# Kernel tuning notes

Measured on AMD Instinct MI355X. Metric: run time of the kernel, lower is better.

Reference implementation:

```python
import jax, jax.numpy as jnp
import numpy as np

B, N, E, R = 2, 4096, 1024, 128   # batch, seq_len, embed_dim, expand_ratio (head_dim)
H = E // R                        # num heads (scalar decay per head)
EPS = 1e-5                        # torch LayerNorm default eps


def _silu(x):
    return x * jax.nn.sigmoid(x)


def setup_inputs() -> dict:
    key = jax.random.key(0)
    ks = jax.random.split(key, 12)
    std = 0.02

    def w(k, shape):
        return jax.random.normal(k, shape, jnp.float32) * std

    return {
        "x": jax.random.normal(ks[0], (B, N, E), jnp.float32),
        # log of lower bound of the decay gate; must be negative so exp() in (0,1)
        "log_lower_bound": -jax.random.uniform(ks[1], (H,), jnp.float32, minval=0.1, maxval=3.0),
        "Wq": w(ks[2], (E, E)),
        "Wk": w(ks[3], (E, E)),
        "Wv": w(ks[4], (E, E)),
        "Wf": w(ks[5], (H, E)),      # f_proj: embed_dim -> embed_dim // expand_ratio
        "Wb1": w(ks[6], (R, E)),     # bet_proj low-rank
        "Wb2": w(ks[7], (E, R)),
        "Wg1": w(ks[8], (R, E)),     # output_gate low-rank
        "Wg2": w(ks[9], (E, R)),
        "gamma": jnp.ones((E,), jnp.float32),  # LayerNorm weight (bias=False)
        "Wo": w(ks[10], (E, E)),
    }


def _simple_gla(q, k, v, g):
    """Gated linear attention recurrence (fla simple_gla semantics).
    q,k,v: [B,H,N,R]; g: [B,H,N] (log decay per head per step).
    S_t = exp(g_t) * S_{t-1} + k_t v_t^T ;  o_t = (q_t * d^-0.5) @ S_t
    """
    scale = q.shape[-1] ** -0.5
    qT = jnp.moveaxis(q, 2, 0)  # [N,B,H,R]
    kT = jnp.moveaxis(k, 2, 0)
    vT = jnp.moveaxis(v, 2, 0)
    gT = jnp.moveaxis(g, 2, 0)  # [N,B,H]

    S0 = jnp.zeros((q.shape[0], q.shape[1], q.shape[-1], v.shape[-1]), q.dtype)

    def step(S, inp):
        qt, kt, vt, gt = inp
        S = S * jnp.exp(gt)[..., None, None] + kt[..., :, None] * vt[..., None, :]
        o = jnp.einsum('bhk,bhkv->bhv', qt * scale, S)
        return S, o

    _, o = jax.lax.scan(step, S0, (qT, kT, vT, gT))
    return jnp.moveaxis(o, 0, 2)  # [B,H,N,R]


def reference(x, log_lower_bound, Wq, Wk, Wv, Wf, Wb1, Wb2, Wg1, Wg2, gamma, Wo):
    # projections + activations
    q = _silu(x @ Wq.T)
    k = _silu(x @ Wk.T)
    v = x @ Wv.T
    f = x @ Wf.T                      # [B,N,H] scalar decay logits per head

    # householder q-transform with dense-memory beta (normalized reflection vector)
    beta = _silu((x @ Wb1.T) @ Wb2.T)  # [B,N,E]
    bn = beta * jax.lax.rsqrt(jnp.sum(beta * beta, -1, keepdims=True) + 1e-12)
    q = q - 2.0 * jnp.sum(q * bn, -1, keepdims=True) * bn

    def split_heads(t):  # [B,N,E] -> [B,H,N,R]
        return jnp.moveaxis(t.reshape(B, N, H, R), 2, 1)

    qh, kh, vh = split_heads(q), split_heads(k), split_heads(v)

    # log-space decay gate with lower bound
    lb = jnp.exp(log_lower_bound)                      # [H] in (0,1)
    fg = lb + (1.0 - lb) * jax.nn.sigmoid(f)           # [B,N,H]
    log_f = jnp.transpose(jnp.log(fg), (0, 2, 1))      # [B,H,N]

    o = _simple_gla(qh, kh, vh, log_f)                 # [B,H,N,R]
    o = jnp.moveaxis(o, 1, 2).reshape(B, N, E)

    # output gate
    gate = jax.nn.sigmoid((x @ Wg1.T) @ Wg2.T)
    o = o * gate

    # LayerNorm (weight only, bias=False)
    mu = jnp.mean(o, -1, keepdims=True)
    var = jnp.mean((o - mu) ** 2, -1, keepdims=True)
    o = (o - mu) * jax.lax.rsqrt(var + EPS) * gamma

    return o @ Wo.T
```

## Files before the change

kernel.cpp:

```cpp
#include <hip/hip_runtime.h>
#include <hip/hip_bf16.h>

using u16 = unsigned short;
typedef __attribute__((ext_vector_type(8))) short bf16x8;
typedef __attribute__((ext_vector_type(4))) float f32x4;
typedef __attribute__((ext_vector_type(8))) u16 u16x8;
typedef __attribute__((ext_vector_type(4))) u16 u16x4;

#define B_ 2
#define N_ 4096
#define E_ 1024
#define R_ 128
#define H_ 8
#define M_ 8192
#define CHUNK_ 128
#define NC_ 32
#define BH_ 16

__device__ __forceinline__ float b2f(u16 u) { return __uint_as_float(((unsigned)u) << 16); }
__device__ __forceinline__ u16 f2b(float f) {
  unsigned u = __float_as_uint(f);
  return (u16)((u + 0x7fffu + ((u >> 16) & 1u)) >> 16);
}
__device__ __forceinline__ float sigm(float x) {
  return __builtin_amdgcn_rcpf(1.0f + __expf(-x));
}

#define GLDS(g, l) __builtin_amdgcn_global_load_lds( \
    (const __attribute__((address_space(1))) unsigned int*)(g), \
    (__attribute__((address_space(3))) unsigned int*)(l), 16, 0, 0)

struct CvtArgs {
  const float* src[10];
  u16* dst[11];
};

__global__ void __launch_bounds__(256) cvt_all(CvtArgs a) {
  int idx = blockIdx.x * 256 + threadIdx.x;
  const int SZ[11] = {2097152, 262144, 262144, 262144, 2048,
                      32768, 32768, 32768, 32768, 262144, 30720};
  int off = idx, seg = 0;
#pragma unroll
  for (int i = 0; i < 10; i++) {
    if (seg == i && off >= SZ[i]) { off -= SZ[i]; seg = i + 1; }
  }
  u16x4 z = (u16x4){0, 0, 0, 0};
  if (seg == 10) { ((u16x4*)a.dst[10])[off] = z; return; }
  float4 v = ((const float4*)a.src[seg])[off];
  u16x4 r;
  r[0] = f2b(v.x); r[1] = f2b(v.y); r[2] = f2b(v.z); r[3] = f2b(v.w);
  if (seg == 6) {
    int n = off >> 5, c = off & 31;
    u16x4* W2 = (u16x4*)a.dst[6];
    W2[n * 64 + c] = r; W2[n * 64 + 32 + c] = z;
  } else if (seg == 8) {
    int n = off >> 5, c = off & 31;
    u16x4* W2 = (u16x4*)a.dst[8];
    W2[(1024 + n) * 64 + 32 + c] = r; W2[(1024 + n) * 64 + c] = z;
  } else {
    ((u16x4*)a.dst[seg])[off] = r;
  }
}

template<bool SWAP>
__device__ __forceinline__ void mfma_panel(f32x4 (&acc)[4][4], const u16* A, const u16* Bm,
                                           int wr, int wc, int l15, int q8) {
  bf16x8 af[4], bf[4];
#pragma unroll
  for (int mi = 0; mi < 4; mi++) af[mi] = *(const bf16x8*)&A[(wr * 64 + mi * 16 + l15) * 32 + q8];
#pragma unroll
  for (int ni = 0; ni < 4; ni++) bf[ni] = *(const bf16x8*)&Bm[(wc * 64 + ni * 16 + l15) * 32 + q8];
#pragma unroll
  for (int mi = 0; mi < 4; mi++)
#pragma unroll
    for (int ni = 0; ni < 4; ni++)
      acc[mi][ni] = SWAP
        ? __builtin_amdgcn_mfma_f32_16x16x32_bf16(bf[ni], af[mi], acc[mi][ni], 0, 0, 0)
        : __builtin_amdgcn_mfma_f32_16x16x32_bf16(af[mi], bf[ni], acc[mi][ni], 0, 0, 0);
}

template<bool SWAP, int K>
__device__ __forceinline__ void gemm_loop(const u16* __restrict__ X, const u16* __restrict__ W,
                                          int m0, int n0,
                                          u16* As, u16* Bs, f32x4 (&acc)[4][4], int tid) {
  const int wave = tid >> 6, lane = tid & 63;
  const int wr = wave >> 1, wc = wave & 1, l15 = lane & 15, q8 = (lane >> 4) * 8;
  const u16* Ap = X + (size_t)(m0 + wave * 32 + (lane >> 2)) * K + (lane & 3) * 8;
  const u16* Bp = W + (size_t)(n0 + wave * 32 + (lane >> 2)) * K + (lane & 3) * 8;
  u16* A0 = As + wave * 1024;
  u16* B0 = Bs + wave * 1024;
#pragma unroll
  for (int k0 = 0; k0 < K; k0 += 64) {
    GLDS(Ap + k0,                    A0);
    GLDS(Ap + 16 * (size_t)K + k0,   A0 + 512);
    GLDS(Ap + k0 + 32,               A0 + 4096);
    GLDS(Ap + 16 * (size_t)K + k0 + 32, A0 + 4608);
    GLDS(Bp + k0,                    B0);
    GLDS(Bp + 16 * (size_t)K + k0,   B0 + 512);
    GLDS(Bp + k0 + 32,               B0 + 4096);
    GLDS(Bp + 16 * (size_t)K + k0 + 32, B0 + 4608);
    __syncthreads();
    mfma_panel<SWAP>(acc, As, Bs, wr, wc, l15, q8);
    mfma_panel<SWAP>(acc, As + 4096, Bs + 4096, wr, wc, l15, q8);
    __syncthreads();
  }
}

template<bool SWAP>
__device__ __forceinline__ void gemm128_dbuf(const u16* __restrict__ X, const u16* __restrict__ W,
                                             int m0, int n0, u16* sh, f32x4 (&acc)[4][4], int tid) {
  const int w = tid >> 6, lane = tid & 63;
  const int wr = w >> 1, wc = w & 1;
  const int l15 = lane & 15, g = lane >> 4;
  const int lrow = tid >> 2;
  const int scol = (tid & 3) ^ ((lrow ^ (lrow >> 2)) & 3);
  const u16* pA0 = X + (size_t)(m0 + lrow) * 1024 + scol * 8;
  const u16* pA1 = X + (size_t)(m0 + 64 + lrow) * 1024 + scol * 8;
  const u16* pB0 = W + (size_t)(n0 + lrow) * 1024 + scol * 8;
  const u16* pB1 = W + (size_t)(n0 + 64 + lrow) * 1024 + scol * 8;
  const int sw = (g ^ (l15 & 3) ^ ((l15 >> 2) & 3)) << 4;
  const int abase = (wr * 64 + l15) * 64 + sw;
  const int bbase = (wc * 64 + l15) * 64 + sw;

#define STG128(T, bi) do {                                                      \
    char* Ad_ = (char*)sh + (bi) * 16384;                                       \
    char* Bd_ = (char*)sh + 8192 + (bi) * 16384;                                \
    GLDS(pA0 + (size_t)(T) * 32, Ad_ + w * 1024);                               \
    GLDS(pA1 + (size_t)(T) * 32, Ad_ + 4096 + w * 1024);                        \
    GLDS(pB0 + (size_t)(T) * 32, Bd_ + w * 1024);                               \
    GLDS(pB1 + (size_t)(T) * 32, Bd_ + 4096 + w * 1024);                        \
  } while (0)

  STG128(0, 0);
  __syncthreads();

#pragma unroll 2
  for (int t = 0; t < 32; ++t) {
    if (t < 31) STG128(t + 1, (t + 1) & 1);
    const char* Ab = (const char*)sh + (t & 1) * 16384;
    const char* Bb = (const char*)sh + 8192 + (t & 1) * 16384;
    bf16x8 af[4], bf[4];
#pragma unroll
    for (int mi = 0; mi < 4; mi++) af[mi] = *(const bf16x8*)(Ab + abase + mi * 1024);
#pragma unroll
    for (int ni = 0; ni < 4; ni++) bf[ni] = *(const bf16x8*)(Bb + bbase + ni * 1024);
    __builtin_amdgcn_s_setprio(1);
#pragma unroll
    for (int mi = 0; mi < 4; mi++)
#pragma unroll
      for (int ni = 0; ni < 4; ni++)
        acc[mi][ni] = SWAP
          ? __builtin_amdgcn_mfma_f32_16x16x32_bf16(bf[ni], af[mi], acc[mi][ni], 0, 0, 0)
          : __builtin_amdgcn_mfma_f32_16x16x32_bf16(af[mi], bf[ni], acc[mi][ni], 0, 0, 0);
    __builtin_amdgcn_s_setprio(0);
    __syncthreads();
  }
#undef STG128
}

__global__ void __launch_bounds__(256, 4) mega_gemm(const u16* __restrict__ X, const u16* __restrict__ Wcat,
                                                    const float* __restrict__ llb,
                                                    u16* __restrict__ Qb, u16* __restrict__ Kb,
                                                    u16* __restrict__ KT, u16* __restrict__ VT,
                                                    u16* __restrict__ T1, float* __restrict__ LOGF) {
  __shared__ u16 sh[17408];
  u16* Ts = sh;
  const int tid = threadIdx.x;
  const int m0 = blockIdx.y * 128;
  const int ny = blockIdx.x, n0 = ny * 128;
  const int wave = tid >> 6, lane = tid & 63;
  const int wr = wave >> 1, wc = wave & 1, l15 = lane & 15, q4 = (lane >> 4) * 4;
  f32x4 acc[4][4];
#pragma unroll
  for (int i = 0; i < 4; i++)
#pragma unroll
    for (int j = 0; j < 4; j++) acc[i][j] = (f32x4){0.f, 0.f, 0.f, 0.f};

  if (ny >= 16 && ny < 24) {
    gemm128_dbuf<false>(X, Wcat, m0, n0, sh, acc, tid);
#pragma unroll
    for (int mi = 0; mi < 4; mi++) {
#pragma unroll
      for (int ni = 0; ni < 4; ni++) {
        int col = n0 - 2048 + wc * 64 + ni * 16 + l15;
        int rbase = m0 + wr * 64 + mi * 16 + q4;
        int head = col >> 7, rl = col & 127;
        int bb = rbase >> 12, nseq = rbase & (N_ - 1);
        u16x4 pk;
#pragma unroll
        for (int r = 0; r < 4; r++) pk[r] = f2b(acc[mi][ni][r]);
        *(u16x4*)&VT[((size_t)(bb * H_ + head) * R_ + rl) * N_ + nseq] = pk;
      }
    }
    return;
  }

  gemm128_dbuf<true>(X, Wcat, m0, n0, sh, acc, tid);

  if (ny == 26) {
    if (wc == 0 && (lane >> 4) < 2) {
#pragma unroll
      for (int mi = 0; mi < 4; mi++) {
        int mcol = m0 + wr * 64 + mi * 16 + l15;
        int bb = mcol >> 12, nseq = mcol & (N_ - 1);
#pragma unroll
        for (int r = 0; r < 4; r++) {
          int h = q4 + r;
          float lb = __expf(llb[h]);
          LOGF[(size_t)(bb * H_ + h) * N_ + nseq] =
              __logf(lb + (1.f - lb) * sigm(acc[mi][0][r]));
        }
      }
    }
    return;
  }

#pragma unroll
  for (int mi = 0; mi < 4; mi++) {
#pragma unroll
    for (int ni = 0; ni < 4; ni++) {
      int nb = n0 + wc * 64 + ni * 16 + q4;
      int mcol = m0 + wr * 64 + mi * 16 + l15;
      u16x4 pk;
#pragma unroll
      for (int r = 0; r < 4; r++) {
        float v = acc[mi][ni][r];
        if (ny < 16) v = v * sigm(v);
        pk[r] = f2b(v);
      }
      if (ny < 8) {
        *(u16x4*)&Qb[(size_t)mcol * E_ + nb] = pk;
      } else if (ny < 16) {
        *(u16x4*)&Kb[(size_t)mcol * E_ + nb - 1024] = pk;
        int nl = nb - n0;
        int ml = mcol - m0;
#pragma unroll
        for (int r = 0; r < 4; r++) Ts[(nl + r) * 136 + ml] = pk[r];
      } else {
        *(u16x4*)&T1[(size_t)mcol * 256 + nb - 3072] = pk;
      }
    }
  }

  if (ny >= 8 && ny < 16) {
    __syncthreads();
    int head = (n0 - 1024) >> 7;
    int bb = m0 >> 12, nloc = m0 & (N_ - 1);
    size_t base = ((size_t)(bb * H_ + head) * R_) * N_ + nloc;
#pragma unroll
    for (int p = 0; p < 8; p++) {
      int nl = p * 16 + (tid >> 4);
      int m8 = (tid & 15) * 8;
      u16x8 v = *(const u16x8*)&Ts[nl * 136 + m8];
      *(u16x8*)&KT[base + (size_t)nl * N_ + m8] = v;
    }
  }
}

__global__ void __launch_bounds__(256) bg_gemm(const u16* __restrict__ T1, const u16* __restrict__ W2,
                                               u16* __restrict__ BETA, u16* __restrict__ GATE) {
  __shared__ u16 As[8192];
  __shared__ u16 Bs[8192];
  const int tid = threadIdx.x;
  const int m0 = blockIdx.x * 128;
  const int n0 = blockIdx.y * 128;
  f32x4 acc[4][4];
#pragma unroll
  for (int i = 0; i < 4; i++)
#pragma unroll
    for (int j = 0; j < 4; j++) acc[i][j] = (f32x4){0.f, 0.f, 0.f, 0.f};
  gemm_loop<true, 256>(T1, W2, m0, n0, As, Bs, acc, tid);
  const int wave = tid >> 6, lane = tid & 63;
  const int wr = wave >> 1, wc = wave & 1, l15 = lane & 15, q4 = (lane >> 4) * 4;
#pragma unroll
  for (int mi = 0; mi < 4; mi++) {
#pragma unroll
    for (int ni = 0; ni < 4; ni++) {
      int nb = n0 + wc * 64 + ni * 16 + q4;
      int mcol = m0 + wr * 64 + mi * 16 + l15;
      u16x4 pk;
      if (nb < 1024) {
#pragma unroll
        for (int r = 0; r < 4; r++) {
          float v = acc[mi][ni][r];
          pk[r] = f2b(v * sigm(v));
        }
        *(u16x4*)&BETA[(size_t)mcol * E_ + nb] = pk;
      } else {
#pragma unroll
        for (int r = 0; r < 4; r++) pk[r] = f2b(sigm(acc[mi][ni][r]));
        *(u16x4*)&GATE[(size_t)mcol * E_ + nb - 1024] = pk;
      }
    }
  }
}

__global__ void __launch_bounds__(256) out_gemm(const u16* __restrict__ X, const u16* __restrict__ W,
                                                float* __restrict__ C) {
  __shared__ u16 As[8192];
  __shared__ u16 Bs[8192];
  const int tid = threadIdx.x;
  const int m0 = blockIdx.x * 128;
  const int n0 = blockIdx.y * 128;
  f32x4 acc[4][4];
#pragma unroll
  for (int i = 0; i < 4; i++)
#pragma unroll
    for (int j = 0; j < 4; j++) acc[i][j] = (f32x4){0.f, 0.f, 0.f, 0.f};
  gemm_loop<true, 1024>(X, W, m0, n0, As, Bs, acc, tid);
  const int wave = tid >> 6, lane = tid & 63;
  const int wr = wave >> 1, wc = wave & 1, l15 = lane & 15, q4 = (lane >> 4) * 4;
#pragma unroll
  for (int mi = 0; mi < 4; mi++) {
#pragma unroll
    for (int ni = 0; ni < 4; ni++) {
      int nb = n0 + wc * 64 + ni * 16 + q4;
      int mcol = m0 + wr * 64 + mi * 16 + l15;
      *(f32x4*)&C[(size_t)mcol * E_ + nb] = acc[mi][ni];
    }
  }
}

__global__ void __launch_bounds__(256) householder(u16* __restrict__ Q, const u16* __restrict__ BETA) {
  int row = blockIdx.x;
  int tid = threadIdx.x;
  u16* q = Q + (size_t)row * E_;
  const u16* bt = BETA + (size_t)row * E_;
  u16x4 q4 = *(const u16x4*)(q + tid * 4);
  u16x4 b4 = *(const u16x4*)(bt + tid * 4);
  float qv[4], bv[4];
#pragma unroll
  for (int i = 0; i < 4; i++) { qv[i] = b2f(q4[i]); bv[i] = b2f(b4[i]); }
  float ss = bv[0]*bv[0] + bv[1]*bv[1] + bv[2]*bv[2] + bv[3]*bv[3];
  float qd = qv[0]*bv[0] + qv[1]*bv[1] + qv[2]*bv[2] + qv[3]*bv[3];
  __shared__ float red[8];
#pragma unroll
  for (int m = 1; m < 64; m <<= 1) { ss += __shfl_xor(ss, m); qd += __shfl_xor(qd, m); }
  int wid = tid >> 6;
  if ((tid & 63) == 0) { red[wid] = ss; red[4 + wid] = qd; }
  __syncthreads();
  ss = red[0] + red[1] + red[2] + red[3];
  qd = red[4] + red[5] + red[6] + red[7];
  float coef = 2.f * qd / (ss + 1e-12f);
  const float scale = 0.08838834764831845f;
  u16x4 o4;
#pragma unroll
  for (int i = 0; i < 4; i++) o4[i] = f2b((qv[i] - coef * bv[i]) * scale);
  *(u16x4*)(q + tid * 4) = o4;
}

__device__ __forceinline__ void scan_chunk(const float* __restrict__ lf, float* cum, int tid) {
  if (tid < 64) {
    float a = lf[tid], b = lf[tid + 64];
#pragma unroll
    for (int off = 1; off < 64; off <<= 1) {
      float t = __shfl_up(a, off);  if (tid >= off) a += t;
      float t2 = __shfl_up(b, off); if (tid >= off) b += t2;
    }
    b += __shfl(a, 63);
    cum[tid] = a; cum[tid + 64] = b;
  }
  __syncthreads();
}

__device__ __forceinline__ void stage32(u16* dst, const u16* src, size_t stride, int tid) {
  int r0 = tid >> 2, c8 = (tid & 3) * 8;
  *(u16x8*)&dst[(size_t)r0 * 40 + c8] = *(const u16x8*)&src[(size_t)r0 * stride + c8];
  int r1 = r0 + 64;
  *(u16x8*)&dst[(size_t)r1 * 40 + c8] = *(const u16x8*)&src[(size_t)r1 * stride + c8];
}

__device__ __forceinline__ void stage32_scaled(u16* dst, const u16* src, size_t stride,
                                               const float* w, int j0, int tid) {
  int c8 = (tid & 3) * 8;
  float wv[8];
#pragma unroll
  for (int i = 0; i < 8; i++) wv[i] = w[j0 + c8 + i];
#pragma unroll
  for (int rr = 0; rr < 128; rr += 64) {
    int r = rr + (tid >> 2);
    u16x8 raw = *(const u16x8*)&src[(size_t)r * stride + c8];
    u16x8 o;
#pragma unroll
    for (int i = 0; i < 8; i++) o[i] = f2b(b2f(raw[i]) * wv[i]);
    *(u16x8*)&dst[(size_t)r * 40 + c8] = o;
  }
}

template<bool SWAP>
__device__ __forceinline__ void mfma16(f32x4 (&acc)[4][4], const u16* A, const u16* Bm,
                                       int wr, int wc, int l15, int q8) {
  bf16x8 af[4], bf[4];
#pragma unroll
  for (int mi = 0; mi < 4; mi++) af[mi] = *(const bf16x8*)&A[(wr * 64 + mi * 16 + l15) * 40 + q8];
#pragma unroll
  for (int ni = 0; ni < 4; ni++) bf[ni] = *(const bf16x8*)&Bm[(wc * 64 + ni * 16 + l15) * 40 + q8];
#pragma unroll
  for (int mi = 0; mi < 4; mi++)
#pragma unroll
    for (int ni = 0; ni < 4; ni++)
      acc[mi][ni] = SWAP
        ? __builtin_amdgcn_mfma_f32_16x16x32_bf16(bf[ni], af[mi], acc[mi][ni], 0, 0, 0)
        : __builtin_amdgcn_mfma_f32_16x16x32_bf16(af[mi], bf[ni], acc[mi][ni], 0, 0, 0);
}

__global__ void __launch_bounds__(256) gla_phaseA(const u16* __restrict__ KT, const u16* __restrict__ VT,
                                                  const float* __restrict__ LOGF,
                                                  u16* __restrict__ U, float* __restrict__ DC) {
  const int blk = blockIdx.x;
  const int bh = blk >> 5, c = blk & 31;
  const int tid = threadIdx.x;
  const int wave = tid >> 6, lane = tid & 63;
  const int wr = wave >> 1, wc = wave & 1, l15 = lane & 15, q8 = (lane >> 4) * 8;
  __shared__ u16 SA[128 * 40];
  __shared__ u16 SB[128 * 40];
  __shared__ float cum[CHUNK_];
  __shared__ float wd[CHUNK_];
  scan_chunk(LOGF + (size_t)bh * N_ + c * CHUNK_, cum, tid);
  if (tid < 128) wd[tid] = __expf(cum[127] - cum[tid]);
  __syncthreads();
  const u16* vbase = VT + ((size_t)bh * R_) * N_ + (size_t)c * CHUNK_;
  const u16* kbase = KT + ((size_t)bh * R_) * N_ + (size_t)c * CHUNK_;
  f32x4 acc[4][4];
#pragma unroll
  for (int i = 0; i < 4; i++)
#pragma unroll
    for (int j = 0; j < 4; j++) acc[i][j] = (f32x4){0.f, 0.f, 0.f, 0.f};
  for (int j0 = 0; j0 < CHUNK_; j0 += 32) {
    __syncthreads();
    stage32(SA, vbase + j0, N_, tid);
    stage32_scaled(SB, kbase + j0, N_, wd, j0, tid);
    __syncthreads();
    mfma16<true>(acc, SA, SB, wr, wc, l15, q8);
  }
  u16* Up = U + (size_t)blk * (R_ * R_);
  const int q4 = (lane >> 4) * 4;
#pragma unroll
  for (int mi = 0; mi < 4; mi++) {
#pragma unroll
    for (int ni = 0; ni < 4; ni++) {
      int v = wr * 64 + mi * 16 + l15;
      int kb = wc * 64 + ni * 16 + q4;
      u16x4 pk;
#pragma unroll
      for (int r = 0; r < 4; r++) pk[r] = f2b(acc[mi][ni][r]);
      *(u16x4*)&Up[(size_t)v * R_ + kb] = pk;
    }
  }
  if (tid == 0) DC[blk] = __expf(cum[127]);
}

__global__ void __launch_bounds__(256) gla_phaseB(const u16* __restrict__ U, const float* __restrict__ DC,
                                                  u16* __restrict__ SSb) {
  int idx = blockIdx.x * 256 + threadIdx.x;
  int bh = idx >> 14;
  int e = idx & 16383;
  float s = 0.f;
  for (int c = 0; c < NC_; c++) {
    size_t off = ((size_t)bh * NC_ + c) * 16384 + e;
    SSb[off] = f2b(s);
    s = DC[bh * NC_ + c] * s + b2f(U[off]);
  }
}

__global__ void __launch_bounds__(256) gla_phaseC(const u16* __restrict__ Qb, const u16* __restrict__ Kb,
                                                  const u16* __restrict__ VT, const u16* __restrict__ SSb,
                                                  const float* __restrict__ LOGF, u16* __restrict__ Ob) {
  const int blk = blockIdx.x;
  const int bh = blk >> 5, c = blk & 31;
  const int b = bh >> 3, h = bh & 7;
  const int tid = threadIdx.x;
  const int wave = tid >> 6, lane = tid & 63;
  const int wr = wave >> 1, wc = wave & 1, l15 = lane & 15;
  const int q4i = (lane >> 4) * 4, q8 = (lane >> 4) * 8;
  __shared__ u16 SA[128 * 40];
  __shared__ u16 SB[128 * 40];
  __shared__ u16 Ps[128 * 136];
  __shared__ float cum[CHUNK_];
  __shared__ float cumE[CHUNK_];
  scan_chunk(LOGF + (size_t)bh * N_ + c * CHUNK_, cum, tid);
  if (tid < 128) cumE[tid] = __expf(cum[tid]);
  __syncthreads();
  const size_t rowbase = ((size_t)(b * N_ + c * CHUNK_)) * E_ + (size_t)h * R_;
  const u16* vtbase = VT + ((size_t)bh * R_) * N_ + (size_t)c * CHUNK_;
  const u16* ssbase = SSb + (size_t)blk * (R_ * R_);

  f32x4 acc[4][4];
#pragma unroll
  for (int i = 0; i < 4; i++)
#pragma unroll
    for (int j = 0; j < 4; j++) acc[i][j] = (f32x4){0.f, 0.f, 0.f, 0.f};

  for (int r0 = 0; r0 < R_; r0 += 32) {
    __syncthreads();
    stage32(SA, Kb + rowbase + r0, E_, tid);
    stage32(SB, Qb + rowbase + r0, E_, tid);
    __syncthreads();
    mfma16<false>(acc, SA, SB, wr, wc, l15, q8);
  }
#pragma unroll
  for (int mi = 0; mi < 4; mi++) {
#pragma unroll
    for (int ni = 0; ni < 4; ni++) {
      int jb = wr * 64 + mi * 16 + q4i;
      int i = wc * 64 + ni * 16 + l15;
      float ci = cum[i];
      float4 cj = *(const float4*)&cum[jb];
      u16x4 pk;
      float cjv[4] = {cj.x, cj.y, cj.z, cj.w};
#pragma unroll
      for (int r = 0; r < 4; r++) {
        int j = jb + r;
        float w = (j <= i) ? __expf(ci - cjv[r]) : 0.f;
        pk[r] = f2b(acc[mi][ni][r] * w);
      }
      *(u16x4*)&Ps[i * 136 + jb] = pk;
    }
  }
#pragma unroll
  for (int i = 0; i < 4; i++)
#pragma unroll
    for (int j = 0; j < 4; j++) acc[i][j] = (f32x4){0.f, 0.f, 0.f, 0.f};
  for (int k0 = 0; k0 < R_; k0 += 32) {
    __syncthreads();
    stage32(SA, Qb + rowbase + k0, E_, tid);
    stage32(SB, ssbase + k0, R_, tid);
    __syncthreads();
    mfma16<true>(acc, SA, SB, wr, wc, l15, q8);
  }
#pragma unroll
  for (int mi = 0; mi < 4; mi++) {
    float ei = cumE[wr * 64 + mi * 16 + l15];
#pragma unroll
    for (int ni = 0; ni < 4; ni++)
#pragma unroll
      for (int r = 0; r < 4; r++) acc[mi][ni][r] *= ei;
  }
  for (int j0 = 0; j0 < CHUNK_; j0 += 32) {
    __syncthreads();
    stage32(SB, vtbase + j0, N_, tid);
    __syncthreads();
    if (wr == 1 || j0 < 64) {
      bf16x8 af[4], bf[4];
#pragma unroll
      for (int mi = 0; mi < 4; mi++)
        af[mi] = *(const bf16x8*)&Ps[(wr * 64 + mi * 16 + l15) * 136 + j0 + q8];
#pragma unroll
      for (int ni = 0; ni < 4; ni++)
        bf[ni] = *(const bf16x8*)&SB[(wc * 64 + ni * 16 + l15) * 40 + q8];
#pragma unroll
      for (int mi = 0; mi < 4; mi++)
#pragma unroll
        for (int ni = 0; ni < 4; ni++)
          acc[mi][ni] = __builtin_amdgcn_mfma_f32_16x16x32_bf16(bf[ni], af[mi], acc[mi][ni], 0, 0, 0);
    }
  }
#pragma unroll
  for (int mi = 0; mi < 4; mi++) {
#pragma unroll
    for (int ni = 0; ni < 4; ni++) {
      int i = wr * 64 + mi * 16 + l15;
      int vb = wc * 64 + ni * 16 + q4i;
      u16x4 pk;
#pragma unroll
      for (int r = 0; r < 4; r++) pk[r] = f2b(acc[mi][ni][r]);
      *(u16x4*)&Ob[rowbase + (size_t)i * E_ + vb] = pk;
    }
  }
}

__global__ void __launch_bounds__(256) gate_ln(const u16* __restrict__ O, const u16* __restrict__ G,
                                               const float* __restrict__ gamma, u16* __restrict__ OLN) {
  int row = blockIdx.x, tid = threadIdx.x;
  u16x4 o4 = *(const u16x4*)(O + (size_t)row * E_ + tid * 4);
  u16x4 g4 = *(const u16x4*)(G + (size_t)row * E_ + tid * 4);
  float x0 = b2f(o4[0]) * b2f(g4[0]), x1 = b2f(o4[1]) * b2f(g4[1]);
  float x2 = b2f(o4[2]) * b2f(g4[2]), x3 = b2f(o4[3]) * b2f(g4[3]);
  float s = x0 + x1 + x2 + x3;
  float sq = x0 * x0 + x1 * x1 + x2 * x2 + x3 * x3;
  __shared__ float red[8];
#pragma unroll
  for (int m = 1; m < 64; m <<= 1) { s += __shfl_xor(s, m); sq += __shfl_xor(sq, m); }
  int wid = tid >> 6;
  if ((tid & 63) == 0) { red[wid] = s; red[4 + wid] = sq; }
  __syncthreads();
  s = red[0] + red[1] + red[2] + red[3];
  sq = red[4] + red[5] + red[6] + red[7];
  float mu = s * (1.f / 1024.f);
  float var = sq * (1.f / 1024.f) - mu * mu;
  float rs = rsqrtf(var + 1e-5f);
  int e = tid * 4;
  u16x4 r4;
  r4[0] = f2b((x0 - mu) * rs * gamma[e + 0]);
  r4[1] = f2b((x1 - mu) * rs * gamma[e + 1]);
  r4[2] = f2b((x2 - mu) * rs * gamma[e + 2]);
  r4[3] = f2b((x3 - mu) * rs * gamma[e + 3]);
  *(u16x4*)(OLN + (size_t)row * E_ + e) = r4;
}

extern "C" void kernel_launch(void* const* d_in, const int* in_sizes, int n_in,
                              void* d_out, int out_size, void* d_ws, size_t ws_size,
                              hipStream_t stream) {
  (void)in_sizes; (void)n_in; (void)out_size; (void)ws_size;
  const float* x   = (const float*)d_in[0];
  const float* llb = (const float*)d_in[1];
  const float* Wq  = (const float*)d_in[2];
  const float* Wk  = (const float*)d_in[3];
  const float* Wv  = (const float*)d_in[4];
  const float* Wf  = (const float*)d_in[5];
  const float* Wb1 = (const float*)d_in[6];
  const float* Wb2 = (const float*)d_in[7];
  const float* Wg1 = (const float*)d_in[8];
  const float* Wg2 = (const float*)d_in[9];
  const float* gm  = (const float*)d_in[10];
  const float* Wo  = (const float*)d_in[11];
  float* out = (float*)d_out;

  char* ws = (char*)d_ws;
  const size_t SZB = (size_t)M_ * E_ * 2;
  u16*   Qb    = (u16*)(ws + 0 * SZB);
  u16*   Kb    = (u16*)(ws + 1 * SZB);
  u16*   KT    = (u16*)(ws + 2 * SZB);
  u16*   VT    = (u16*)(ws + 3 * SZB);
  u16*   BETAb = (u16*)(ws + 4 * SZB);
  u16*   GATEb = (u16*)(ws + 5 * SZB);
  u16*   SSb   = (u16*)(ws + 6 * SZB);
  u16*   XB    = (u16*)(ws + 7 * SZB);
  u16*   U     = (u16*)(ws + 8 * SZB);
  char*  tail  = ws + 8 * SZB + (size_t)BH_ * NC_ * R_ * R_ * 2;
  u16*   Wcat  = (u16*)tail;
  u16*   Wcat2 = Wcat + (size_t)3456 * 1024;
  u16*   WOb   = Wcat2 + (size_t)2048 * 256;
  u16*   T1    = WOb + (size_t)E_ * E_;
  float* LOGF  = (float*)(T1 + (size_t)M_ * 256);
  float* DC    = LOGF + (size_t)BH_ * N_;
  u16*   Ob    = BETAb;
  u16*   OLN   = Qb;

  CvtArgs ca;
  ca.src[0] = x;   ca.dst[0]  = XB;
  ca.src[1] = Wq;  ca.dst[1]  = Wcat;
  ca.src[2] = Wk;  ca.dst[2]  = Wcat + (size_t)1024 * 1024;
  ca.src[3] = Wv;  ca.dst[3]  = Wcat + (size_t)2048 * 1024;
  ca.src[4] = Wf;  ca.dst[4]  = Wcat + (size_t)3328 * 1024;
  ca.src[5] = Wb1; ca.dst[5]  = Wcat + (size_t)3072 * 1024;
  ca.src[6] = Wb2; ca.dst[6]  = Wcat2;
  ca.src[7] = Wg1; ca.dst[7]  = Wcat + (size_t)3200 * 1024;
  ca.src[8] = Wg2; ca.dst[8]  = Wcat2;
  ca.src[9] = Wo;  ca.dst[9]  = WOb;
  ca.dst[10] = Wcat + (size_t)3336 * 1024;

  dim3 blk(256);
  cvt_all<<<dim3(12928), blk, 0, stream>>>(ca);
  mega_gemm<<<dim3(27, 64), blk, 0, stream>>>(XB, Wcat, llb, Qb, Kb, KT, VT, T1, LOGF);
  bg_gemm<<<dim3(64, 16), blk, 0, stream>>>(T1, Wcat2, BETAb, GATEb);
  householder<<<dim3(M_), blk, 0, stream>>>(Qb, BETAb);
  gla_phaseA<<<dim3(BH_ * NC_), blk, 0, stream>>>(KT, VT, LOGF, U, DC);
  gla_phaseB<<<dim3(BH_ * 16384 / 256), blk, 0, stream>>>(U, DC, SSb);
  gla_phaseC<<<dim3(BH_ * NC_), blk, 0, stream>>>(Qb, Kb, VT, SSb, LOGF, Ob);
  gate_ln<<<dim3(M_), blk, 0, stream>>>(Ob, GATEb, gm, OLN);
  out_gemm<<<dim3(64, 8), blk, 0, stream>>>(OLN, WOb, out);
}
```

Before: 310.1 us.

## Swap GEMM loops between kernels and double-buffer chunk-attention staging

Makes the double-buffered 128-tile GEMM generic over K and uses it in bg_gemm and out_gemm, each now tagged with an occupancy hint of 4. mega_gemm goes back to the simpler single-buffered gemm_loop and loses its occupancy hint. The chunk-state and chunk-output kernels now stage their 32-wide slices into two alternating shared buffers, so the next slice's global load overlaps the current MFMA work and one barrier per step is removed. The cost is more shared memory per block in the attention kernels, which may lower occupancy, and mega_gemm no longer overlaps its loads with compute.

```diff
diff --git a/kernel.cpp b/kernel.cpp
--- a/kernel.cpp
+++ b/kernel.cpp
@@ -106,7 +106,7 @@
   }
 }
 
-template<bool SWAP>
+template<bool SWAP, int K>
 __device__ __forceinline__ void gemm128_dbuf(const u16* __restrict__ X, const u16* __restrict__ W,
                                              int m0, int n0, u16* sh, f32x4 (&acc)[4][4], int tid) {
   const int w = tid >> 6, lane = tid & 63;
@@ -114,10 +114,10 @@
   const int l15 = lane & 15, g = lane >> 4;
   const int lrow = tid >> 2;
   const int scol = (tid & 3) ^ ((lrow ^ (lrow >> 2)) & 3);
-  const u16* pA0 = X + (size_t)(m0 + lrow) * 1024 + scol * 8;
-  const u16* pA1 = X + (size_t)(m0 + 64 + lrow) * 1024 + scol * 8;
-  const u16* pB0 = W + (size_t)(n0 + lrow) * 1024 + scol * 8;
-  const u16* pB1 = W + (size_t)(n0 + 64 + lrow) * 1024 + scol * 8;
+  const u16* pA0 = X + (size_t)(m0 + lrow) * K + scol * 8;
+  const u16* pA1 = X + (size_t)(m0 + 64 + lrow) * K + scol * 8;
+  const u16* pB0 = W + (size_t)(n0 + lrow) * K + scol * 8;
+  const u16* pB1 = W + (size_t)(n0 + 64 + lrow) * K + scol * 8;
   const int sw = (g ^ (l15 & 3) ^ ((l15 >> 2) & 3)) << 4;
   const int abase = (wr * 64 + l15) * 64 + sw;
   const int bbase = (wc * 64 + l15) * 64 + sw;
@@ -135,8 +135,8 @@
   __syncthreads();
 
 #pragma unroll 2
-  for (int t = 0; t < 32; ++t) {
-    if (t < 31) STG128(t + 1, (t + 1) & 1);
+  for (int t = 0; t < K / 32; ++t) {
+    if (t < K / 32 - 1) STG128(t + 1, (t + 1) & 1);
     const char* Ab = (const char*)sh + (t & 1) * 16384;
     const char* Bb = (const char*)sh + 8192 + (t & 1) * 16384;
     bf16x8 af[4], bf[4];
@@ -158,12 +158,14 @@
 #undef STG128
 }
 
-__global__ void __launch_bounds__(256, 4) mega_gemm(const u16* __restrict__ X, const u16* __restrict__ Wcat,
-                                                    const float* __restrict__ llb,
-                                                    u16* __restrict__ Qb, u16* __restrict__ Kb,
-                                                    u16* __restrict__ KT, u16* __restrict__ VT,
-                                                    u16* __restrict__ T1, float* __restrict__ LOGF) {
+__global__ void __launch_bounds__(256) mega_gemm(const u16* __restrict__ X, const u16* __restrict__ Wcat,
+                                                 const float* __restrict__ llb,
+                                                 u16* __restrict__ Qb, u16* __restrict__ Kb,
+                                                 u16* __restrict__ KT, u16* __restrict__ VT,
+                                                 u16* __restrict__ T1, float* __restrict__ LOGF) {
   __shared__ u16 sh[17408];
+  u16* As = sh;
+  u16* Bs = sh + 8192;
   u16* Ts = sh;
   const int tid = threadIdx.x;
   const int m0 = blockIdx.y * 128;
@@ -177,7 +179,7 @@
     for (int j = 0; j < 4; j++) acc[i][j] = (f32x4){0.f, 0.f, 0.f, 0.f};
 
   if (ny >= 16 && ny < 24) {
-    gemm128_dbuf<false>(X, Wcat, m0, n0, sh, acc, tid);
+    gemm_loop<false, 1024>(X, Wcat, m0, n0, As, Bs, acc, tid);
 #pragma unroll
     for (int mi = 0; mi < 4; mi++) {
 #pragma unroll
@@ -195,7 +197,7 @@
     return;
   }
 
-  gemm128_dbuf<true>(X, Wcat, m0, n0, sh, acc, tid);
+  gemm_loop<true, 1024>(X, Wcat, m0, n0, As, Bs, acc, tid);
 
   if (ny == 26) {
     if (wc == 0 && (lane >> 4) < 2) {
@@ -257,10 +259,9 @@
   }
 }
 
-__global__ void __launch_bounds__(256) bg_gemm(const u16* __restrict__ T1, const u16* __restrict__ W2,
-                                               u16* __restrict__ BETA, u16* __restrict__ GATE) {
-  __shared__ u16 As[8192];
-  __shared__ u16 Bs[8192];
+__global__ void __launch_bounds__(256, 4) bg_gemm(const u16* __restrict__ T1, const u16* __restrict__ W2,
+                                                  u16* __restrict__ BETA, u16* __restrict__ GATE) {
+  __shared__ u16 sh[16384];
   const int tid = threadIdx.x;
   const int m0 = blockIdx.x * 128;
   const int n0 = blockIdx.y * 128;
@@ -269,7 +270,7 @@
   for (int i = 0; i < 4; i++)
 #pragma unroll
     for (int j = 0; j < 4; j++) acc[i][j] = (f32x4){0.f, 0.f, 0.f, 0.f};
-  gemm_loop<true, 256>(T1, W2, m0, n0, As, Bs, acc, tid);
+  gemm128_dbuf<true, 256>(T1, W2, m0, n0, sh, acc, tid);
   const int wave = tid >> 6, lane = tid & 63;
   const int wr = wave >> 1, wc = wave & 1, l15 = lane & 15, q4 = (lane >> 4) * 4;
 #pragma unroll
@@ -295,10 +296,9 @@
   }
 }
 
-__global__ void __launch_bounds__(256) out_gemm(const u16* __restrict__ X, const u16* __restrict__ W,
-                                                float* __restrict__ C) {
-  __shared__ u16 As[8192];
-  __shared__ u16 Bs[8192];
+__global__ void __launch_bounds__(256, 4) out_gemm(const u16* __restrict__ X, const u16* __restrict__ W,
+                                                   float* __restrict__ C) {
+  __shared__ u16 sh[16384];
   const int tid = threadIdx.x;
   const int m0 = blockIdx.x * 128;
   const int n0 = blockIdx.y * 128;
@@ -307,7 +307,7 @@
   for (int i = 0; i < 4; i++)
 #pragma unroll
     for (int j = 0; j < 4; j++) acc[i][j] = (f32x4){0.f, 0.f, 0.f, 0.f};
-  gemm_loop<true, 1024>(X, W, m0, n0, As, Bs, acc, tid);
+  gemm128_dbuf<true, 1024>(X, W, m0, n0, sh, acc, tid);
   const int wave = tid >> 6, lane = tid & 63;
   const int wr = wave >> 1, wc = wave & 1, l15 = lane & 15, q4 = (lane >> 4) * 4;
 #pragma unroll
@@ -412,8 +412,8 @@
   const int tid = threadIdx.x;
   const int wave = tid >> 6, lane = tid & 63;
   const int wr = wave >> 1, wc = wave & 1, l15 = lane & 15, q8 = (lane >> 4) * 8;
-  __shared__ u16 SA[128 * 40];
-  __shared__ u16 SB[128 * 40];
+  __shared__ u16 SA[2][128 * 40];
+  __shared__ u16 SB[2][128 * 40];
   __shared__ float cum[CHUNK_];
   __shared__ float wd[CHUNK_];
   scan_chunk(LOGF + (size_t)bh * N_ + c * CHUNK_, cum, tid);
@@ -426,12 +426,17 @@
   for (int i = 0; i < 4; i++)
 #pragma unroll
     for (int j = 0; j < 4; j++) acc[i][j] = (f32x4){0.f, 0.f, 0.f, 0.f};
-  for (int j0 = 0; j0 < CHUNK_; j0 += 32) {
-    __syncthreads();
-    stage32(SA, vbase + j0, N_, tid);
-    stage32_scaled(SB, kbase + j0, N_, wd, j0, tid);
-    __syncthreads();
-    mfma16<true>(acc, SA, SB, wr, wc, l15, q8);
+  stage32(SA[0], vbase, N_, tid);
+  stage32_scaled(SB[0], kbase, N_, wd, 0, tid);
+  __syncthreads();
+#pragma unroll
+  for (int j = 0; j < 4; j++) {
+    if (j < 3) {
+      stage32(SA[(j + 1) & 1], vbase + (j + 1) * 32, N_, tid);
+      stage32_scaled(SB[(j + 1) & 1], kbase + (j + 1) * 32, N_, wd, (j + 1) * 32, tid);
+    }
+    mfma16<true>(acc, SA[j & 1], SB[j & 1], wr, wc, l15, q8);
+    __syncthreads();
   }
   u16* Up = U + (size_t)blk * (R_ * R_);
   const int q4 = (lane >> 4) * 4;
@@ -473,8 +478,8 @@
   const int wave = tid >> 6, lane = tid & 63;
   const int wr = wave >> 1, wc = wave & 1, l15 = lane & 15;
   const int q4i = (lane >> 4) * 4, q8 = (lane >> 4) * 8;
-  __shared__ u16 SA[128 * 40];
-  __shared__ u16 SB[128 * 40];
+  __shared__ u16 SA[2][128 * 40];
+  __shared__ u16 SB[2][128 * 40];
   __shared__ u16 Ps[128 * 136];
   __shared__ float cum[CHUNK_];
   __shared__ float cumE[CHUNK_];
@@ -491,12 +496,17 @@
 #pragma unroll
     for (int j = 0; j < 4; j++) acc[i][j] = (f32x4){0.f, 0.f, 0.f, 0.f};
 
-  for (int r0 = 0; r0 < R_; r0 += 32) {
-    __syncthreads();
-    stage32(SA, Kb + rowbase + r0, E_, tid);
-    stage32(SB, Qb + rowbase + r0, E_, tid);
-    __syncthreads();
-    mfma16<false>(acc, SA, SB, wr, wc, l15, q8);
+  stage32(SA[0], Kb + rowbase, E_, tid);
+  stage32(SB[0], Qb + rowbase, E_, tid);
+  __syncthreads();
+#pragma unroll
+  for (int r = 0; r < 4; r++) {
+    if (r < 3) {
+      stage32(SA[(r + 1) & 1], Kb + rowbase + (r + 1) * 32, E_, tid);
+      stage32(SB[(r + 1) & 1], Qb + rowbase + (r + 1) * 32, E_, tid);
+    }
+    mfma16<false>(acc, SA[r & 1], SB[r & 1], wr, wc, l15, q8);
+    __syncthreads();
   }
 #pragma unroll
   for (int mi = 0; mi < 4; mi++) {
@@ -521,12 +531,18 @@
   for (int i = 0; i < 4; i++)
 #pragma unroll
     for (int j = 0; j < 4; j++) acc[i][j] = (f32x4){0.f, 0.f, 0.f, 0.f};
-  for (int k0 = 0; k0 < R_; k0 += 32) {
-    __syncthreads();
-    stage32(SA, Qb + rowbase + k0, E_, tid);
-    stage32(SB, ssbase + k0, R_, tid);
-    __syncthreads();
-    mfma16<true>(acc, SA, SB, wr, wc, l15, q8);
+  __syncthreads();
+  stage32(SA[0], Qb + rowbase, E_, tid);
+  stage32(SB[0], ssbase, R_, tid);
+  __syncthreads();
+#pragma unroll
+  for (int k = 0; k < 4; k++) {
+    if (k < 3) {
+      stage32(SA[(k + 1) & 1], Qb + rowbase + (k + 1) * 32, E_, tid);
+      stage32(SB[(k + 1) & 1], ssbase + (k + 1) * 32, R_, tid);
+    }
+    mfma16<true>(acc, SA[k & 1], SB[k & 1], wr, wc, l15, q8);
+    __syncthreads();
   }
 #pragma unroll
   for (int mi = 0; mi < 4; mi++) {
@@ -536,10 +552,12 @@
 #pragma unroll
       for (int r = 0; r < 4; r++) acc[mi][ni][r] *= ei;
   }
-  for (int j0 = 0; j0 < CHUNK_; j0 += 32) {
-    __syncthreads();
-    stage32(SB, vtbase + j0, N_, tid);
-    __syncthreads();
+  stage32(SB[0], vtbase, N_, tid);
+  __syncthreads();
+#pragma unroll
+  for (int j = 0; j < 4; j++) {
+    int j0 = j * 32;
+    if (j < 3) stage32(SB[(j + 1) & 1], vtbase + (j + 1) * 32, N_, tid);
     if (wr == 1 || j0 < 64) {
       bf16x8 af[4], bf[4];
 #pragma unroll
@@ -547,13 +565,14 @@
         af[mi] = *(const bf16x8*)&Ps[(wr * 64 + mi * 16 + l15) * 136 + j0 + q8];
 #pragma unroll
       for (int ni = 0; ni < 4; ni++)
-        bf[ni] = *(const bf16x8*)&SB[(wc * 64 + ni * 16 + l15) * 40 + q8];
+        bf[ni] = *(const bf16x8*)&SB[j & 1][(wc * 64 + ni * 16 + l15) * 40 + q8];
 #pragma unroll
       for (int mi = 0; mi < 4; mi++)
 #pragma unroll
         for (int ni = 0; ni < 4; ni++)
           acc[mi][ni] = __builtin_amdgcn_mfma_f32_16x16x32_bf16(bf[ni], af[mi], acc[mi][ni], 0, 0, 0);
     }
+    __syncthreads();
   }
 #pragma unroll
   for (int mi = 0; mi < 4; mi++) {
```

Result: no change. 313.1 us (+1.0%).
